# Optimization experiments

Hardware: AMD Instinct MI355X
Metric: run time of the kernel (lower is better)

## Reference

```python
import jax, jax.numpy as jnp
import numpy as np

B, D, H = 1024, 64, 128


def setup_inputs() -> dict:
    key = jax.random.key(0)
    ks = jax.random.split(key, 12)
    s1 = 1.0 / np.sqrt(4 * D)
    sh = 1.0 / np.sqrt(H)
    sd = 1.0 / np.sqrt(D)
    return {
        "x": jax.random.normal(ks[0], (B, D), dtype=jnp.float32),
        # edge_fn: Linear(4D,H) -> ReLU -> Linear(H,H)
        "W1": jax.random.uniform(ks[1], (4 * D, H), minval=-s1, maxval=s1, dtype=jnp.float32),
        "b1": jax.random.uniform(ks[2], (H,), minval=-s1, maxval=s1, dtype=jnp.float32),
        "W2": jax.random.uniform(ks[3], (H, H), minval=-sh, maxval=sh, dtype=jnp.float32),
        "b2": jax.random.uniform(ks[4], (H,), minval=-sh, maxval=sh, dtype=jnp.float32),
        # tau_proj: Linear(D,1) -> Softplus
        "Wt": jax.random.uniform(ks[5], (D, 1), minval=-sd, maxval=sd, dtype=jnp.float32),
        "bt": jax.random.uniform(ks[6], (1,), minval=-sd, maxval=sd, dtype=jnp.float32),
        # agg: Linear(H,H) -> ReLU
        "Wa": jax.random.uniform(ks[7], (H, H), minval=-sh, maxval=sh, dtype=jnp.float32),
        "ba": jax.random.uniform(ks[8], (H,), minval=-sh, maxval=sh, dtype=jnp.float32),
        # res_proj: Linear(D,H)
        "Wr": jax.random.uniform(ks[9], (D, H), minval=-sd, maxval=sd, dtype=jnp.float32),
        "br": jax.random.uniform(ks[10], (H,), minval=-sd, maxval=sd, dtype=jnp.float32),
        # LayerNorm(H)
        "gamma": jnp.ones((H,), dtype=jnp.float32),
        "beta": jnp.zeros((H,), dtype=jnp.float32),
    }


def reference(x, W1, b1, W2, b2, Wt, bt, Wa, ba, Wr, br, gamma, beta):
    d = x.shape[1]
    # Decompose first linear over concat([x_i, x_j, delta, |delta|]) into 4 sub-matmuls;
    # only the |delta| term needs the pairwise [B,B,D] tensor.
    Wi, Wj, Wd, Wab = W1[:d], W1[d:2 * d], W1[2 * d:3 * d], W1[3 * d:]
    ti = x @ Wi            # [B,H] (i-dependent)
    tj = x @ Wj            # [B,H] (j-dependent)
    td = x @ Wd            # [B,H] (delta = x_i - x_j contribution)
    delta = x[:, None, :] - x[None, :, :]             # [B,B,D]
    ta = jnp.einsum('ijd,dh->ijh', jnp.abs(delta), Wab)  # [B,B,H]
    pre = ti[:, None, :] + tj[None, :, :] + td[:, None, :] - td[None, :, :] + ta + b1
    d_proj = jax.nn.relu(pre) @ W2 + b2               # [B,B,H]
    tau = jnp.maximum(jax.nn.softplus(x @ Wt + bt), 0.01) + 1.0  # [B,1]
    h_mean = d_proj.mean(axis=1) / tau                # mean over j
    h = jax.nn.relu(h_mean @ Wa + ba)
    y = h + (x @ Wr + br)
    mu = y.mean(axis=-1, keepdims=True)
    var = ((y - mu) ** 2).mean(axis=-1, keepdims=True)  # biased, like torch LayerNorm
    return (y - mu) * jax.lax.rsqrt(var + 1e-5) * gamma + beta
```

## Files before the change

kernel.cpp:

```cpp
#include <hip/hip_runtime.h>
#include <hip/hip_bf16.h>
#include <math.h>

#define BB 1024
#define DD 64
#define HH 128

typedef __bf16 bf16x8 __attribute__((ext_vector_type(8)));
typedef float floatx4 __attribute__((ext_vector_type(4)));

__device__ __forceinline__ unsigned short f2bf(float v) {
    union { float f; unsigned u; } a; a.f = v;
    unsigned r = a.u + 0x7fffu + ((a.u >> 16) & 1u);
    return (unsigned short)(r >> 16);
}

__device__ __forceinline__ void async_cp16(const float* g, float* lds_wave_base) {
    __builtin_amdgcn_global_load_lds(
        (const __attribute__((address_space(1))) unsigned int*)g,
        (__attribute__((address_space(3))) unsigned int*)lds_wave_base,
        16, 0, 0);
}

__global__ __launch_bounds__(256) void prep_kernel(
    const float* __restrict__ x, const float* __restrict__ W1,
    const float* __restrict__ b1,
    float* __restrict__ c1, float* __restrict__ c2P,
    unsigned short* __restrict__ wpack)
{
    __shared__ float xs[8][DD];
    const int t = threadIdx.x;
    const int i0 = blockIdx.x * 8;
    xs[t >> 6][t & 63] = x[i0 * DD + t];
    xs[4 + (t >> 6)][t & 63] = x[i0 * DD + 256 + t];
    __syncthreads();

    const int ii = t >> 5;
    const int h4 = t & 31;
    const int h = h4 * 4;
    const int i = i0 + ii;

    float4 a1 = {0.f, 0.f, 0.f, 0.f};
    float4 a2 = {0.f, 0.f, 0.f, 0.f};
    #pragma unroll 4
    for (int k = 0; k < DD; k++) {
        float4 wi = *(const float4*)(W1 + k * HH + h);
        float4 wj = *(const float4*)(W1 + (DD + k) * HH + h);
        float4 wd = *(const float4*)(W1 + (2 * DD + k) * HH + h);
        float xv = xs[ii][k];
        a1.x = fmaf(xv, wi.x + wd.x, a1.x);
        a1.y = fmaf(xv, wi.y + wd.y, a1.y);
        a1.z = fmaf(xv, wi.z + wd.z, a1.z);
        a1.w = fmaf(xv, wi.w + wd.w, a1.w);
        a2.x = fmaf(xv, wj.x - wd.x, a2.x);
        a2.y = fmaf(xv, wj.y - wd.y, a2.y);
        a2.z = fmaf(xv, wj.z - wd.z, a2.z);
        a2.w = fmaf(xv, wj.w - wd.w, a2.w);
    }
    float4 b1v = *(const float4*)(b1 + h);
    float4 c1v = {a1.x + b1v.x, a1.y + b1v.y, a1.z + b1v.z, a1.w + b1v.w};
    *(float4*)(c1 + i * HH + h) = c1v;

    const int jl = i & 15;
    float* cb = c2P + (i >> 4) * 2048 + (h >> 4) * 256 + (jl & 3);
    const int p0 = ((jl >> 2) * 16 + (h & 15));
    cb[(p0 + 0) * 4] = a2.x;
    cb[(p0 + 1) * 4] = a2.y;
    cb[(p0 + 2) * 4] = a2.z;
    cb[(p0 + 3) * 4] = a2.w;

    if (blockIdx.x < 64) {
        int f = blockIdx.x * 256 + t;
        int jj = f & 7, l = (f >> 3) & 63, u = f >> 9;
        int s = u & 1, t8 = u >> 1;
        int k = s * 32 + ((l >> 4) << 3) + jj;
        int hh = t8 * 16 + (l & 15);
        wpack[f] = f2bf(W1[(3 * DD + k) * HH + hh]);
    }
}

__global__ __launch_bounds__(256) void pair_kernel(
    const float* __restrict__ x, const float* __restrict__ c1,
    const float* __restrict__ c2P, const unsigned short* __restrict__ wpack,
    float* __restrict__ Sp)
{
    __shared__ __align__(16) float xs[2][1024];
    __shared__ __align__(16) float c2s[2][2048];

    const int t = threadIdx.x;
    const int wave = t >> 6;
    const int l = t & 63;
    const int quad = l >> 4, lm = l & 15;
    const int ig = blockIdx.x >> 2;
    const int jq = blockIdx.x & 3;
    const int i = ig * 4 + wave;
    const int j0base = jq * 256;
    const int sw = lm & 7;

    async_cp16(x + (j0base + (t >> 4)) * DD + (((t & 15) ^ ((t >> 4) & 7)) << 2),
               &xs[0][0] + wave * 256);
    {
        const float* cg = c2P + (j0base >> 4) * 2048;
        async_cp16(cg + t * 4,        &c2s[0][0]    + wave * 256);
        async_cp16(cg + 1024 + t * 4, &c2s[0][1024] + wave * 256);
    }

    float xi[16];
    {
        const float* xg = x + i * DD + quad * 8;
        *(float4*)(xi)      = *(const float4*)(xg);
        *(float4*)(xi + 4)  = *(const float4*)(xg + 4);
        *(float4*)(xi + 8)  = *(const float4*)(xg + 32);
        *(float4*)(xi + 12) = *(const float4*)(xg + 36);
    }
    float c1r[8];
    #pragma unroll
    for (int t8 = 0; t8 < 8; t8++) c1r[t8] = c1[i * HH + t8 * 16 + lm];
    bf16x8 wf[16];
    #pragma unroll
    for (int u = 0; u < 16; u++)
        wf[u] = *(const bf16x8*)(wpack + (u * 64 + l) * 8);

    float S[8];
    #pragma unroll
    for (int t8 = 0; t8 < 8; t8++) S[t8] = 0.f;

    for (int tile = 0; tile < 16; ++tile) {
        const int cur = tile & 1;
        __syncthreads();

        if (tile < 15) {
            const int jn = j0base + (tile + 1) * 16;
            async_cp16(x + (jn + (t >> 4)) * DD + (((t & 15) ^ ((t >> 4) & 7)) << 2),
                       &xs[cur ^ 1][0] + wave * 256);
            const float* cg = c2P + (jn >> 4) * 2048;
            async_cp16(cg + t * 4,        &c2s[cur ^ 1][0]    + wave * 256);
            async_cp16(cg + 1024 + t * 4, &c2s[cur ^ 1][1024] + wave * 256);
        }

        floatx4 acc[8];
        #pragma unroll
        for (int t8 = 0; t8 < 8; t8++) {
            float4 c2v = *(const float4*)(&c2s[cur][t8 * 256 + l * 4]);
            acc[t8][0] = c2v.x + c1r[t8];
            acc[t8][1] = c2v.y + c1r[t8];
            acc[t8][2] = c2v.z + c1r[t8];
            acc[t8][3] = c2v.w + c1r[t8];
        }

        const float* xb = &xs[cur][lm * 64];
        float4 a0 = *(const float4*)(xb + (((quad * 2)     ^ sw) << 2));
        float4 a1 = *(const float4*)(xb + (((quad * 2 + 1) ^ sw) << 2));
        float4 a2 = *(const float4*)(xb + (((quad * 2 + 8) ^ sw) << 2));
        float4 a3 = *(const float4*)(xb + (((quad * 2 + 9) ^ sw) << 2));
        bf16x8 af0, af1;
        af0[0] = (__bf16)fabsf(xi[0] - a0.x);  af0[1] = (__bf16)fabsf(xi[1] - a0.y);
        af0[2] = (__bf16)fabsf(xi[2] - a0.z);  af0[3] = (__bf16)fabsf(xi[3] - a0.w);
        af0[4] = (__bf16)fabsf(xi[4] - a1.x);  af0[5] = (__bf16)fabsf(xi[5] - a1.y);
        af0[6] = (__bf16)fabsf(xi[6] - a1.z);  af0[7] = (__bf16)fabsf(xi[7] - a1.w);
        af1[0] = (__bf16)fabsf(xi[8] - a2.x);  af1[1] = (__bf16)fabsf(xi[9] - a2.y);
        af1[2] = (__bf16)fabsf(xi[10] - a2.z); af1[3] = (__bf16)fabsf(xi[11] - a2.w);
        af1[4] = (__bf16)fabsf(xi[12] - a3.x); af1[5] = (__bf16)fabsf(xi[13] - a3.y);
        af1[6] = (__bf16)fabsf(xi[14] - a3.z); af1[7] = (__bf16)fabsf(xi[15] - a3.w);

        #pragma unroll
        for (int t8 = 0; t8 < 8; t8++) {
            acc[t8] = __builtin_amdgcn_mfma_f32_16x16x32_bf16(af0, wf[t8 * 2 + 0], acc[t8], 0, 0, 0);
            acc[t8] = __builtin_amdgcn_mfma_f32_16x16x32_bf16(af1, wf[t8 * 2 + 1], acc[t8], 0, 0, 0);
        }
        #pragma unroll
        for (int t8 = 0; t8 < 8; t8++) {
            S[t8] += fmaxf(acc[t8][0], 0.f);
            S[t8] += fmaxf(acc[t8][1], 0.f);
            S[t8] += fmaxf(acc[t8][2], 0.f);
            S[t8] += fmaxf(acc[t8][3], 0.f);
        }
    }

    #pragma unroll
    for (int t8 = 0; t8 < 8; t8++) {
        S[t8] += __shfl_xor(S[t8], 16, 64);
        S[t8] += __shfl_xor(S[t8], 32, 64);
    }
    if (quad == 0) {
        #pragma unroll
        for (int t8 = 0; t8 < 8; t8++)
            Sp[(jq * BB + i) * HH + t8 * 16 + lm] = S[t8];
    }
}

__global__ __launch_bounds__(256) void finish_kernel(
    const float* __restrict__ Sp, const float* __restrict__ W2,
    const float* __restrict__ b2, const float* __restrict__ x,
    const float* __restrict__ Wt, const float* __restrict__ bt,
    const float* __restrict__ Wa, const float* __restrict__ ba,
    const float* __restrict__ Wr, const float* __restrict__ br,
    const float* __restrict__ gamma, const float* __restrict__ beta,
    float* __restrict__ out)
{
    __shared__ float Srow[8][HH];
    __shared__ float mrow[8][HH];
    __shared__ float xrow[8][DD];
    __shared__ float taus[8];
    const int t = threadIdx.x;
    const int ii = t >> 5;
    const int h4 = t & 31;
    const int h = h4 * 4;
    const int i0 = blockIdx.x * 8;
    const int i = i0 + ii;

    {
        float4 s = {0.f, 0.f, 0.f, 0.f};
        #pragma unroll
        for (int q = 0; q < 4; q++) {
            float4 v = *(const float4*)(Sp + (q * BB + i) * HH + h);
            s.x += v.x; s.y += v.y; s.z += v.z; s.w += v.w;
        }
        const float inv = 1.0f / (float)BB;
        float4 sm = {s.x * inv, s.y * inv, s.z * inv, s.w * inv};
        *(float4*)(&Srow[ii][h]) = sm;
    }
    xrow[t >> 6][t & 63] = x[i0 * DD + t];
    xrow[4 + (t >> 6)][t & 63] = x[i0 * DD + 256 + t];

    {
        float p = x[i * DD + h4] * Wt[h4] + x[i * DD + 32 + h4] * Wt[32 + h4];
        #pragma unroll
        for (int off = 16; off; off >>= 1) p += __shfl_xor(p, off, 64);
        if (h4 == 0) {
            float z = p + bt[0];
            float sp = (z > 20.f) ? z : log1pf(expf(z));
            taus[ii] = fmaxf(sp, 0.01f) + 1.0f;
        }
    }
    __syncthreads();

    float4 acc = *(const float4*)(b2 + h);
    #pragma unroll 8
    for (int k = 0; k < HH; k++) {
        float4 w = *(const float4*)(W2 + k * HH + h);
        float sv = Srow[ii][k];
        acc.x = fmaf(sv, w.x, acc.x); acc.y = fmaf(sv, w.y, acc.y);
        acc.z = fmaf(sv, w.z, acc.z); acc.w = fmaf(sv, w.w, acc.w);
    }
    const float itau = 1.0f / taus[ii];
    float4 mv = {acc.x * itau, acc.y * itau, acc.z * itau, acc.w * itau};
    *(float4*)(&mrow[ii][h]) = mv;
    __syncthreads();

    float4 a2 = *(const float4*)(ba + h);
    #pragma unroll 8
    for (int k = 0; k < HH; k++) {
        float4 w = *(const float4*)(Wa + k * HH + h);
        float sv = mrow[ii][k];
        a2.x = fmaf(sv, w.x, a2.x); a2.y = fmaf(sv, w.y, a2.y);
        a2.z = fmaf(sv, w.z, a2.z); a2.w = fmaf(sv, w.w, a2.w);
    }
    float4 brv = *(const float4*)(br + h);
    float4 y = {fmaxf(a2.x, 0.f) + brv.x, fmaxf(a2.y, 0.f) + brv.y,
                fmaxf(a2.z, 0.f) + brv.z, fmaxf(a2.w, 0.f) + brv.w};
    #pragma unroll 8
    for (int d = 0; d < DD; d++) {
        float4 w = *(const float4*)(Wr + d * HH + h);
        float xv = xrow[ii][d];
        y.x = fmaf(xv, w.x, y.x); y.y = fmaf(xv, w.y, y.y);
        y.z = fmaf(xv, w.z, y.z); y.w = fmaf(xv, w.w, y.w);
    }

    float p = y.x + y.y + y.z + y.w;
    #pragma unroll
    for (int off = 16; off; off >>= 1) p += __shfl_xor(p, off, 64);
    float mu = p * (1.0f / (float)HH);
    float4 dy = {y.x - mu, y.y - mu, y.z - mu, y.w - mu};
    float q = dy.x * dy.x + dy.y * dy.y + dy.z * dy.z + dy.w * dy.w;
    #pragma unroll
    for (int off = 16; off; off >>= 1) q += __shfl_xor(q, off, 64);
    float rs = rsqrtf(q * (1.0f / (float)HH) + 1e-5f);
    float4 gv = *(const float4*)(gamma + h);
    float4 bv = *(const float4*)(beta + h);
    float4 o = {dy.x * rs * gv.x + bv.x, dy.y * rs * gv.y + bv.y,
                dy.z * rs * gv.z + bv.z, dy.w * rs * gv.w + bv.w};
    *(float4*)(out + i * HH + h) = o;
}

extern "C" void kernel_launch(void* const* d_in, const int* in_sizes, int n_in,
                              void* d_out, int out_size, void* d_ws, size_t ws_size,
                              hipStream_t stream)
{
    const float* x     = (const float*)d_in[0];
    const float* W1    = (const float*)d_in[1];
    const float* b1    = (const float*)d_in[2];
    const float* W2    = (const float*)d_in[3];
    const float* b2    = (const float*)d_in[4];
    const float* Wt    = (const float*)d_in[5];
    const float* bt    = (const float*)d_in[6];
    const float* Wa    = (const float*)d_in[7];
    const float* ba    = (const float*)d_in[8];
    const float* Wr    = (const float*)d_in[9];
    const float* br    = (const float*)d_in[10];
    const float* gamma = (const float*)d_in[11];
    const float* beta  = (const float*)d_in[12];
    float* out = (float*)d_out;

    char* ws = (char*)d_ws;
    float*          c1    = (float*)(ws);
    float*          c2P   = (float*)(ws + (512 << 10));
    unsigned short* wpack = (unsigned short*)(ws + (1024 << 10));
    float*          Sp    = (float*)(ws + (1056 << 10));

    prep_kernel<<<128, 256, 0, stream>>>(x, W1, b1, c1, c2P, wpack);
    pair_kernel<<<1024, 256, 0, stream>>>(x, c1, c2P, wpack, Sp);
    finish_kernel<<<128, 256, 0, stream>>>(Sp, W2, b2, x, Wt, bt,
                                           Wa, ba, Wr, br, gamma, beta, out);
}
```

Measured before the change: 147.8 us.

## Fold j-dependent term into MFMA K dimension and drop LDS staging

Instead of precomputing the j-dependent c2 table and staging it through LDS, the pair kernel now widens the MFMA K dimension from 64 to 128, appending x_j against a packed (Wj - Wd) weight so the j-term is computed inside the matrix core. The block split changes from four j-quarters to two j-halves times two H-halves, and x_j rows are read straight from global into registers with manual double buffering, with no LDS and no barriers. This removes the c2P workspace, its scattered writes, async LDS copies and syncs, at the cost of twice as many MFMAs per output and extra bf16 rounding of the x_j term.

```diff
diff --git a/kernel.cpp b/kernel.cpp
--- a/kernel.cpp
+++ b/kernel.cpp
@@ -15,18 +15,10 @@
     return (unsigned short)(r >> 16);
 }
 
-__device__ __forceinline__ void async_cp16(const float* g, float* lds_wave_base) {
-    __builtin_amdgcn_global_load_lds(
-        (const __attribute__((address_space(1))) unsigned int*)g,
-        (__attribute__((address_space(3))) unsigned int*)lds_wave_base,
-        16, 0, 0);
-}
-
 __global__ __launch_bounds__(256) void prep_kernel(
     const float* __restrict__ x, const float* __restrict__ W1,
     const float* __restrict__ b1,
-    float* __restrict__ c1, float* __restrict__ c2P,
-    unsigned short* __restrict__ wpack)
+    float* __restrict__ c1, unsigned short* __restrict__ wpack)
 {
     __shared__ float xs[8][DD];
     const int t = threadIdx.x;
@@ -41,69 +33,88 @@
     const int i = i0 + ii;
 
     float4 a1 = {0.f, 0.f, 0.f, 0.f};
-    float4 a2 = {0.f, 0.f, 0.f, 0.f};
     #pragma unroll 4
     for (int k = 0; k < DD; k++) {
         float4 wi = *(const float4*)(W1 + k * HH + h);
-        float4 wj = *(const float4*)(W1 + (DD + k) * HH + h);
         float4 wd = *(const float4*)(W1 + (2 * DD + k) * HH + h);
         float xv = xs[ii][k];
         a1.x = fmaf(xv, wi.x + wd.x, a1.x);
         a1.y = fmaf(xv, wi.y + wd.y, a1.y);
         a1.z = fmaf(xv, wi.z + wd.z, a1.z);
         a1.w = fmaf(xv, wi.w + wd.w, a1.w);
-        a2.x = fmaf(xv, wj.x - wd.x, a2.x);
-        a2.y = fmaf(xv, wj.y - wd.y, a2.y);
-        a2.z = fmaf(xv, wj.z - wd.z, a2.z);
-        a2.w = fmaf(xv, wj.w - wd.w, a2.w);
     }
     float4 b1v = *(const float4*)(b1 + h);
     float4 c1v = {a1.x + b1v.x, a1.y + b1v.y, a1.z + b1v.z, a1.w + b1v.w};
     *(float4*)(c1 + i * HH + h) = c1v;
 
-    const int jl = i & 15;
-    float* cb = c2P + (i >> 4) * 2048 + (h >> 4) * 256 + (jl & 3);
-    const int p0 = ((jl >> 2) * 16 + (h & 15));
-    cb[(p0 + 0) * 4] = a2.x;
-    cb[(p0 + 1) * 4] = a2.y;
-    cb[(p0 + 2) * 4] = a2.z;
-    cb[(p0 + 3) * 4] = a2.w;
-
     if (blockIdx.x < 64) {
         int f = blockIdx.x * 256 + t;
-        int jj = f & 7, l = (f >> 3) & 63, u = f >> 9;
-        int s = u & 1, t8 = u >> 1;
-        int k = s * 32 + ((l >> 4) << 3) + jj;
-        int hh = t8 * 16 + (l & 15);
-        wpack[f] = f2bf(W1[(3 * DD + k) * HH + hh]);
-    }
-}
+        int jj = f & 7;
+        int l  = (f >> 3) & 63;
+        int u  = f >> 9;
+        int c  = u & 3, t4 = (u >> 2) & 3, hh = u >> 4;
+        int hcol = hh * 64 + t4 * 16 + (l & 15);
+        float val;
+        if (c < 2) {
+            int k = c * 32 + ((l >> 4) << 3) + jj;
+            val = W1[(3 * DD + k) * HH + hcol];
+        } else {
+            int k = (c - 2) * 32 + ((l >> 4) << 3) + jj;
+            val = W1[(DD + k) * HH + hcol] - W1[(2 * DD + k) * HH + hcol];
+        }
+        wpack[f] = f2bf(val);
+    }
+}
+
+#define LOADT(P0, P1, P2, P3, tile) do {                     \
+    const float* rp_ = xrow + ((tile) & 31) * (16 * DD);     \
+    P0 = *(const float4*)(rp_);                              \
+    P1 = *(const float4*)(rp_ + 4);                          \
+    P2 = *(const float4*)(rp_ + 32);                         \
+    P3 = *(const float4*)(rp_ + 36);                         \
+} while (0)
+
+#define COMPT(A0, A1, A2, A3) do {                                            \
+    bf16x8 af0, af1, af2, af3;                                                \
+    af0[0]=(__bf16)fabsf(xi[0]-A0.x);  af0[1]=(__bf16)fabsf(xi[1]-A0.y);      \
+    af0[2]=(__bf16)fabsf(xi[2]-A0.z);  af0[3]=(__bf16)fabsf(xi[3]-A0.w);      \
+    af0[4]=(__bf16)fabsf(xi[4]-A1.x);  af0[5]=(__bf16)fabsf(xi[5]-A1.y);      \
+    af0[6]=(__bf16)fabsf(xi[6]-A1.z);  af0[7]=(__bf16)fabsf(xi[7]-A1.w);      \
+    af1[0]=(__bf16)fabsf(xi[8]-A2.x);  af1[1]=(__bf16)fabsf(xi[9]-A2.y);      \
+    af1[2]=(__bf16)fabsf(xi[10]-A2.z); af1[3]=(__bf16)fabsf(xi[11]-A2.w);     \
+    af1[4]=(__bf16)fabsf(xi[12]-A3.x); af1[5]=(__bf16)fabsf(xi[13]-A3.y);     \
+    af1[6]=(__bf16)fabsf(xi[14]-A3.z); af1[7]=(__bf16)fabsf(xi[15]-A3.w);     \
+    af2[0]=(__bf16)A0.x; af2[1]=(__bf16)A0.y; af2[2]=(__bf16)A0.z;            \
+    af2[3]=(__bf16)A0.w; af2[4]=(__bf16)A1.x; af2[5]=(__bf16)A1.y;            \
+    af2[6]=(__bf16)A1.z; af2[7]=(__bf16)A1.w;                                 \
+    af3[0]=(__bf16)A2.x; af3[1]=(__bf16)A2.y; af3[2]=(__bf16)A2.z;            \
+    af3[3]=(__bf16)A2.w; af3[4]=(__bf16)A3.x; af3[5]=(__bf16)A3.y;            \
+    af3[6]=(__bf16)A3.z; af3[7]=(__bf16)A3.w;                                 \
+    _Pragma("unroll")                                                         \
+    for (int t4 = 0; t4 < 4; t4++) {                                          \
+        floatx4 acc = {c1r[t4], c1r[t4], c1r[t4], c1r[t4]};                   \
+        acc = __builtin_amdgcn_mfma_f32_16x16x32_bf16(af0, wf[t4*4+0], acc, 0,0,0); \
+        acc = __builtin_amdgcn_mfma_f32_16x16x32_bf16(af1, wf[t4*4+1], acc, 0,0,0); \
+        acc = __builtin_amdgcn_mfma_f32_16x16x32_bf16(af2, wf[t4*4+2], acc, 0,0,0); \
+        acc = __builtin_amdgcn_mfma_f32_16x16x32_bf16(af3, wf[t4*4+3], acc, 0,0,0); \
+        S[t4] += fmaxf(acc[0], 0.f) + fmaxf(acc[1], 0.f)                      \
+               + fmaxf(acc[2], 0.f) + fmaxf(acc[3], 0.f);                     \
+    }                                                                         \
+} while (0)
 
 __global__ __launch_bounds__(256) void pair_kernel(
     const float* __restrict__ x, const float* __restrict__ c1,
-    const float* __restrict__ c2P, const unsigned short* __restrict__ wpack,
-    float* __restrict__ Sp)
-{
-    __shared__ __align__(16) float xs[2][1024];
-    __shared__ __align__(16) float c2s[2][2048];
-
+    const unsigned short* __restrict__ wpack, float* __restrict__ Sp)
+{
     const int t = threadIdx.x;
     const int wave = t >> 6;
     const int l = t & 63;
     const int quad = l >> 4, lm = l & 15;
-    const int ig = blockIdx.x >> 2;
-    const int jq = blockIdx.x & 3;
+    const int bid = blockIdx.x;
+    const int ig = bid >> 2;
+    const int hh = (bid >> 1) & 1;
+    const int jh = bid & 1;
     const int i = ig * 4 + wave;
-    const int j0base = jq * 256;
-    const int sw = lm & 7;
-
-    async_cp16(x + (j0base + (t >> 4)) * DD + (((t & 15) ^ ((t >> 4) & 7)) << 2),
-               &xs[0][0] + wave * 256);
-    {
-        const float* cg = c2P + (j0base >> 4) * 2048;
-        async_cp16(cg + t * 4,        &c2s[0][0]    + wave * 256);
-        async_cp16(cg + 1024 + t * 4, &c2s[0][1024] + wave * 256);
-    }
 
     float xi[16];
     {
@@ -113,79 +124,41 @@
         *(float4*)(xi + 8)  = *(const float4*)(xg + 32);
         *(float4*)(xi + 12) = *(const float4*)(xg + 36);
     }
-    float c1r[8];
-    #pragma unroll
-    for (int t8 = 0; t8 < 8; t8++) c1r[t8] = c1[i * HH + t8 * 16 + lm];
+    float c1r[4];
+    #pragma unroll
+    for (int t4 = 0; t4 < 4; t4++)
+        c1r[t4] = c1[i * HH + hh * 64 + t4 * 16 + lm];
+
     bf16x8 wf[16];
     #pragma unroll
     for (int u = 0; u < 16; u++)
-        wf[u] = *(const bf16x8*)(wpack + (u * 64 + l) * 8);
-
-    float S[8];
-    #pragma unroll
-    for (int t8 = 0; t8 < 8; t8++) S[t8] = 0.f;
-
-    for (int tile = 0; tile < 16; ++tile) {
-        const int cur = tile & 1;
-        __syncthreads();
-
-        if (tile < 15) {
-            const int jn = j0base + (tile + 1) * 16;
-            async_cp16(x + (jn + (t >> 4)) * DD + (((t & 15) ^ ((t >> 4) & 7)) << 2),
-                       &xs[cur ^ 1][0] + wave * 256);
-            const float* cg = c2P + (jn >> 4) * 2048;
-            async_cp16(cg + t * 4,        &c2s[cur ^ 1][0]    + wave * 256);
-            async_cp16(cg + 1024 + t * 4, &c2s[cur ^ 1][1024] + wave * 256);
-        }
-
-        floatx4 acc[8];
-        #pragma unroll
-        for (int t8 = 0; t8 < 8; t8++) {
-            float4 c2v = *(const float4*)(&c2s[cur][t8 * 256 + l * 4]);
-            acc[t8][0] = c2v.x + c1r[t8];
-            acc[t8][1] = c2v.y + c1r[t8];
-            acc[t8][2] = c2v.z + c1r[t8];
-            acc[t8][3] = c2v.w + c1r[t8];
-        }
-
-        const float* xb = &xs[cur][lm * 64];
-        float4 a0 = *(const float4*)(xb + (((quad * 2)     ^ sw) << 2));
-        float4 a1 = *(const float4*)(xb + (((quad * 2 + 1) ^ sw) << 2));
-        float4 a2 = *(const float4*)(xb + (((quad * 2 + 8) ^ sw) << 2));
-        float4 a3 = *(const float4*)(xb + (((quad * 2 + 9) ^ sw) << 2));
-        bf16x8 af0, af1;
-        af0[0] = (__bf16)fabsf(xi[0] - a0.x);  af0[1] = (__bf16)fabsf(xi[1] - a0.y);
-        af0[2] = (__bf16)fabsf(xi[2] - a0.z);  af0[3] = (__bf16)fabsf(xi[3] - a0.w);
-        af0[4] = (__bf16)fabsf(xi[4] - a1.x);  af0[5] = (__bf16)fabsf(xi[5] - a1.y);
-        af0[6] = (__bf16)fabsf(xi[6] - a1.z);  af0[7] = (__bf16)fabsf(xi[7] - a1.w);
-        af1[0] = (__bf16)fabsf(xi[8] - a2.x);  af1[1] = (__bf16)fabsf(xi[9] - a2.y);
-        af1[2] = (__bf16)fabsf(xi[10] - a2.z); af1[3] = (__bf16)fabsf(xi[11] - a2.w);
-        af1[4] = (__bf16)fabsf(xi[12] - a3.x); af1[5] = (__bf16)fabsf(xi[13] - a3.y);
-        af1[6] = (__bf16)fabsf(xi[14] - a3.z); af1[7] = (__bf16)fabsf(xi[15] - a3.w);
-
-        #pragma unroll
-        for (int t8 = 0; t8 < 8; t8++) {
-            acc[t8] = __builtin_amdgcn_mfma_f32_16x16x32_bf16(af0, wf[t8 * 2 + 0], acc[t8], 0, 0, 0);
-            acc[t8] = __builtin_amdgcn_mfma_f32_16x16x32_bf16(af1, wf[t8 * 2 + 1], acc[t8], 0, 0, 0);
-        }
-        #pragma unroll
-        for (int t8 = 0; t8 < 8; t8++) {
-            S[t8] += fmaxf(acc[t8][0], 0.f);
-            S[t8] += fmaxf(acc[t8][1], 0.f);
-            S[t8] += fmaxf(acc[t8][2], 0.f);
-            S[t8] += fmaxf(acc[t8][3], 0.f);
-        }
-    }
-
-    #pragma unroll
-    for (int t8 = 0; t8 < 8; t8++) {
-        S[t8] += __shfl_xor(S[t8], 16, 64);
-        S[t8] += __shfl_xor(S[t8], 32, 64);
+        wf[u] = *(const bf16x8*)(wpack + ((hh * 16 + u) * 64 + l) * 8);
+
+    float S[4] = {0.f, 0.f, 0.f, 0.f};
+
+    const float* xrow = x + (jh * 512 + lm) * DD + quad * 8;
+
+    float4 A0, A1, A2, A3, B0, B1, B2, B3;
+    LOADT(A0, A1, A2, A3, 0);
+    LOADT(B0, B1, B2, B3, 1);
+
+    #pragma unroll 1
+    for (int tp = 0; tp < 32; tp += 2) {
+        COMPT(A0, A1, A2, A3);
+        LOADT(A0, A1, A2, A3, tp + 2);
+        COMPT(B0, B1, B2, B3);
+        LOADT(B0, B1, B2, B3, tp + 3);
+    }
+
+    #pragma unroll
+    for (int t4 = 0; t4 < 4; t4++) {
+        S[t4] += __shfl_xor(S[t4], 16, 64);
+        S[t4] += __shfl_xor(S[t4], 32, 64);
     }
     if (quad == 0) {
         #pragma unroll
-        for (int t8 = 0; t8 < 8; t8++)
-            Sp[(jq * BB + i) * HH + t8 * 16 + lm] = S[t8];
+        for (int t4 = 0; t4 < 4; t4++)
+            Sp[(jh * BB + i) * HH + hh * 64 + t4 * 16 + lm] = S[t4];
     }
 }
 
@@ -200,7 +173,7 @@
 {
     __shared__ float Srow[8][HH];
     __shared__ float mrow[8][HH];
-    __shared__ float xrow[8][DD];
+    __shared__ float xrowS[8][DD];
     __shared__ float taus[8];
     const int t = threadIdx.x;
     const int ii = t >> 5;
@@ -212,7 +185,7 @@
     {
         float4 s = {0.f, 0.f, 0.f, 0.f};
         #pragma unroll
-        for (int q = 0; q < 4; q++) {
+        for (int q = 0; q < 2; q++) {
             float4 v = *(const float4*)(Sp + (q * BB + i) * HH + h);
             s.x += v.x; s.y += v.y; s.z += v.z; s.w += v.w;
         }
@@ -220,8 +193,8 @@
         float4 sm = {s.x * inv, s.y * inv, s.z * inv, s.w * inv};
         *(float4*)(&Srow[ii][h]) = sm;
     }
-    xrow[t >> 6][t & 63] = x[i0 * DD + t];
-    xrow[4 + (t >> 6)][t & 63] = x[i0 * DD + 256 + t];
+    xrowS[t >> 6][t & 63] = x[i0 * DD + t];
+    xrowS[4 + (t >> 6)][t & 63] = x[i0 * DD + 256 + t];
 
     {
         float p = x[i * DD + h4] * Wt[h4] + x[i * DD + 32 + h4] * Wt[32 + h4];
@@ -262,7 +235,7 @@
     #pragma unroll 8
     for (int d = 0; d < DD; d++) {
         float4 w = *(const float4*)(Wr + d * HH + h);
-        float xv = xrow[ii][d];
+        float xv = xrowS[ii][d];
         y.x = fmaf(xv, w.x, y.x); y.y = fmaf(xv, w.y, y.y);
         y.z = fmaf(xv, w.z, y.z); y.w = fmaf(xv, w.w, y.w);
     }
@@ -304,12 +277,11 @@
 
     char* ws = (char*)d_ws;
     float*          c1    = (float*)(ws);
-    float*          c2P   = (float*)(ws + (512 << 10));
-    unsigned short* wpack = (unsigned short*)(ws + (1024 << 10));
-    float*          Sp    = (float*)(ws + (1056 << 10));
-
-    prep_kernel<<<128, 256, 0, stream>>>(x, W1, b1, c1, c2P, wpack);
-    pair_kernel<<<1024, 256, 0, stream>>>(x, c1, c2P, wpack, Sp);
+    unsigned short* wpack = (unsigned short*)(ws + (512 << 10));
+    float*          Sp    = (float*)(ws + (576 << 10));
+
+    prep_kernel<<<128, 256, 0, stream>>>(x, W1, b1, c1, wpack);
+    pair_kernel<<<1024, 256, 0, stream>>>(x, c1, wpack, Sp);
     finish_kernel<<<128, 256, 0, stream>>>(Sp, W2, b2, x, Wt, bt,
                                            Wa, ba, Wr, br, gamma, beta, out);
 }
```

After: 245.2 us. +65.8%, slower.

## Split pair kernel over H halves and switch MFMA operands to fp16

Applied to the files above, without the earlier changes.

The pair kernel grid doubles, and each block now handles half of the hidden dimension. That halves per-thread accumulators, weight fragments and LDS for c2, and occupancy is raised with launch_bounds(256,4). The |delta| operands are packed to fp16 with cvt_pkrtz and use the f16 MFMA instead of the bf16 one with per-element conversions, which cuts conversion cost. In exchange, the x tile loads and abs-difference computation are now done twice, once per H half, and the operands use round-toward-zero fp16 conversion.

```diff
diff --git a/kernel.cpp b/kernel.cpp
--- a/kernel.cpp
+++ b/kernel.cpp
@@ -6,14 +6,11 @@
 #define DD 64
 #define HH 128
 
-typedef __bf16 bf16x8 __attribute__((ext_vector_type(8)));
+typedef _Float16 half8 __attribute__((ext_vector_type(8)));
+typedef __fp16 fp16x2 __attribute__((ext_vector_type(2)));
 typedef float floatx4 __attribute__((ext_vector_type(4)));
 
-__device__ __forceinline__ unsigned short f2bf(float v) {
-    union { float f; unsigned u; } a; a.f = v;
-    unsigned r = a.u + 0x7fffu + ((a.u >> 16) & 1u);
-    return (unsigned short)(r >> 16);
-}
+union H8 { fp16x2 p[4]; half8 v; };
 
 __device__ __forceinline__ void async_cp16(const float* g, float* lds_wave_base) {
     __builtin_amdgcn_global_load_lds(
@@ -26,7 +23,7 @@
     const float* __restrict__ x, const float* __restrict__ W1,
     const float* __restrict__ b1,
     float* __restrict__ c1, float* __restrict__ c2P,
-    unsigned short* __restrict__ wpack)
+    _Float16* __restrict__ wpack)
 {
     __shared__ float xs[8][DD];
     const int t = threadIdx.x;
@@ -62,48 +59,49 @@
     *(float4*)(c1 + i * HH + h) = c1v;
 
     const int jl = i & 15;
-    float* cb = c2P + (i >> 4) * 2048 + (h >> 4) * 256 + (jl & 3);
-    const int p0 = ((jl >> 2) * 16 + (h & 15));
+    float* cb = c2P + (i >> 4) * 2048 + (h >> 6) * 1024 + ((h >> 4) & 3) * 256 + (jl & 3);
+    const int p0 = (jl >> 2) * 16 + (h & 15);
     cb[(p0 + 0) * 4] = a2.x;
     cb[(p0 + 1) * 4] = a2.y;
     cb[(p0 + 2) * 4] = a2.z;
     cb[(p0 + 3) * 4] = a2.w;
 
-    if (blockIdx.x < 64) {
+    if (blockIdx.x < 32) {
         int f = blockIdx.x * 256 + t;
-        int jj = f & 7, l = (f >> 3) & 63, u = f >> 9;
-        int s = u & 1, t8 = u >> 1;
-        int k = s * 32 + ((l >> 4) << 3) + jj;
-        int hh = t8 * 16 + (l & 15);
-        wpack[f] = f2bf(W1[(3 * DD + k) * HH + hh]);
-    }
-}
-
-__global__ __launch_bounds__(256) void pair_kernel(
+        int jj = f & 7;
+        int l  = (f >> 3) & 63;
+        int u  = f >> 9;
+        int s  = u & 1, t4 = (u >> 1) & 3, hh = u >> 3;
+        int k  = s * 32 + ((l >> 4) << 3) + jj;
+        int hcol = hh * 64 + t4 * 16 + (l & 15);
+        wpack[f] = (_Float16)W1[(3 * DD + k) * HH + hcol];
+    }
+}
+
+__global__ __launch_bounds__(256, 4) void pair_kernel(
     const float* __restrict__ x, const float* __restrict__ c1,
-    const float* __restrict__ c2P, const unsigned short* __restrict__ wpack,
+    const float* __restrict__ c2P, const _Float16* __restrict__ wpack,
     float* __restrict__ Sp)
 {
     __shared__ __align__(16) float xs[2][1024];
-    __shared__ __align__(16) float c2s[2][2048];
+    __shared__ __align__(16) float c2s[2][1024];
 
     const int t = threadIdx.x;
     const int wave = t >> 6;
     const int l = t & 63;
     const int quad = l >> 4, lm = l & 15;
-    const int ig = blockIdx.x >> 2;
-    const int jq = blockIdx.x & 3;
+    const int bid = blockIdx.x;
+    const int ig = bid >> 3;
+    const int hh = (bid >> 2) & 1;
+    const int jq = bid & 3;
     const int i = ig * 4 + wave;
     const int j0base = jq * 256;
     const int sw = lm & 7;
 
     async_cp16(x + (j0base + (t >> 4)) * DD + (((t & 15) ^ ((t >> 4) & 7)) << 2),
                &xs[0][0] + wave * 256);
-    {
-        const float* cg = c2P + (j0base >> 4) * 2048;
-        async_cp16(cg + t * 4,        &c2s[0][0]    + wave * 256);
-        async_cp16(cg + 1024 + t * 4, &c2s[0][1024] + wave * 256);
-    }
+    async_cp16(c2P + (j0base >> 4) * 2048 + hh * 1024 + t * 4,
+               &c2s[0][0] + wave * 256);
 
     float xi[16];
     {
@@ -113,17 +111,16 @@
         *(float4*)(xi + 8)  = *(const float4*)(xg + 32);
         *(float4*)(xi + 12) = *(const float4*)(xg + 36);
     }
-    float c1r[8];
-    #pragma unroll
-    for (int t8 = 0; t8 < 8; t8++) c1r[t8] = c1[i * HH + t8 * 16 + lm];
-    bf16x8 wf[16];
-    #pragma unroll
-    for (int u = 0; u < 16; u++)
-        wf[u] = *(const bf16x8*)(wpack + (u * 64 + l) * 8);
-
-    float S[8];
-    #pragma unroll
-    for (int t8 = 0; t8 < 8; t8++) S[t8] = 0.f;
+    float c1r[4];
+    #pragma unroll
+    for (int t4 = 0; t4 < 4; t4++)
+        c1r[t4] = c1[i * HH + hh * 64 + t4 * 16 + lm];
+    half8 wf[8];
+    #pragma unroll
+    for (int u = 0; u < 8; u++)
+        wf[u] = *(const half8*)(wpack + ((hh * 8 + u) * 64 + l) * 8);
+
+    float S[4] = {0.f, 0.f, 0.f, 0.f};
 
     for (int tile = 0; tile < 16; ++tile) {
         const int cur = tile & 1;
@@ -133,19 +130,18 @@
             const int jn = j0base + (tile + 1) * 16;
             async_cp16(x + (jn + (t >> 4)) * DD + (((t & 15) ^ ((t >> 4) & 7)) << 2),
                        &xs[cur ^ 1][0] + wave * 256);
-            const float* cg = c2P + (jn >> 4) * 2048;
-            async_cp16(cg + t * 4,        &c2s[cur ^ 1][0]    + wave * 256);
-            async_cp16(cg + 1024 + t * 4, &c2s[cur ^ 1][1024] + wave * 256);
-        }
-
-        floatx4 acc[8];
-        #pragma unroll
-        for (int t8 = 0; t8 < 8; t8++) {
-            float4 c2v = *(const float4*)(&c2s[cur][t8 * 256 + l * 4]);
-            acc[t8][0] = c2v.x + c1r[t8];
-            acc[t8][1] = c2v.y + c1r[t8];
-            acc[t8][2] = c2v.z + c1r[t8];
-            acc[t8][3] = c2v.w + c1r[t8];
+            async_cp16(c2P + (jn >> 4) * 2048 + hh * 1024 + t * 4,
+                       &c2s[cur ^ 1][0] + wave * 256);
+        }
+
+        floatx4 acc[4];
+        #pragma unroll
+        for (int t4 = 0; t4 < 4; t4++) {
+            float4 c2v = *(const float4*)(&c2s[cur][t4 * 256 + l * 4]);
+            acc[t4][0] = c2v.x + c1r[t4];
+            acc[t4][1] = c2v.y + c1r[t4];
+            acc[t4][2] = c2v.z + c1r[t4];
+            acc[t4][3] = c2v.w + c1r[t4];
         }
 
         const float* xb = &xs[cur][lm * 64];
@@ -153,39 +149,39 @@
         float4 a1 = *(const float4*)(xb + (((quad * 2 + 1) ^ sw) << 2));
         float4 a2 = *(const float4*)(xb + (((quad * 2 + 8) ^ sw) << 2));
         float4 a3 = *(const float4*)(xb + (((quad * 2 + 9) ^ sw) << 2));
-        bf16x8 af0, af1;
-        af0[0] = (__bf16)fabsf(xi[0] - a0.x);  af0[1] = (__bf16)fabsf(xi[1] - a0.y);
-        af0[2] = (__bf16)fabsf(xi[2] - a0.z);  af0[3] = (__bf16)fabsf(xi[3] - a0.w);
-        af0[4] = (__bf16)fabsf(xi[4] - a1.x);  af0[5] = (__bf16)fabsf(xi[5] - a1.y);
-        af0[6] = (__bf16)fabsf(xi[6] - a1.z);  af0[7] = (__bf16)fabsf(xi[7] - a1.w);
-        af1[0] = (__bf16)fabsf(xi[8] - a2.x);  af1[1] = (__bf16)fabsf(xi[9] - a2.y);
-        af1[2] = (__bf16)fabsf(xi[10] - a2.z); af1[3] = (__bf16)fabsf(xi[11] - a2.w);
-        af1[4] = (__bf16)fabsf(xi[12] - a3.x); af1[5] = (__bf16)fabsf(xi[13] - a3.y);
-        af1[6] = (__bf16)fabsf(xi[14] - a3.z); af1[7] = (__bf16)fabsf(xi[15] - a3.w);
-
-        #pragma unroll
-        for (int t8 = 0; t8 < 8; t8++) {
-            acc[t8] = __builtin_amdgcn_mfma_f32_16x16x32_bf16(af0, wf[t8 * 2 + 0], acc[t8], 0, 0, 0);
-            acc[t8] = __builtin_amdgcn_mfma_f32_16x16x32_bf16(af1, wf[t8 * 2 + 1], acc[t8], 0, 0, 0);
-        }
-        #pragma unroll
-        for (int t8 = 0; t8 < 8; t8++) {
-            S[t8] += fmaxf(acc[t8][0], 0.f);
-            S[t8] += fmaxf(acc[t8][1], 0.f);
-            S[t8] += fmaxf(acc[t8][2], 0.f);
-            S[t8] += fmaxf(acc[t8][3], 0.f);
-        }
-    }
-
-    #pragma unroll
-    for (int t8 = 0; t8 < 8; t8++) {
-        S[t8] += __shfl_xor(S[t8], 16, 64);
-        S[t8] += __shfl_xor(S[t8], 32, 64);
+        H8 af0, af1;
+        af0.p[0] = __builtin_amdgcn_cvt_pkrtz(fabsf(xi[0] - a0.x),  fabsf(xi[1] - a0.y));
+        af0.p[1] = __builtin_amdgcn_cvt_pkrtz(fabsf(xi[2] - a0.z),  fabsf(xi[3] - a0.w));
+        af0.p[2] = __builtin_amdgcn_cvt_pkrtz(fabsf(xi[4] - a1.x),  fabsf(xi[5] - a1.y));
+        af0.p[3] = __builtin_amdgcn_cvt_pkrtz(fabsf(xi[6] - a1.z),  fabsf(xi[7] - a1.w));
+        af1.p[0] = __builtin_amdgcn_cvt_pkrtz(fabsf(xi[8] - a2.x),  fabsf(xi[9] - a2.y));
+        af1.p[1] = __builtin_amdgcn_cvt_pkrtz(fabsf(xi[10] - a2.z), fabsf(xi[11] - a2.w));
+        af1.p[2] = __builtin_amdgcn_cvt_pkrtz(fabsf(xi[12] - a3.x), fabsf(xi[13] - a3.y));
+        af1.p[3] = __builtin_amdgcn_cvt_pkrtz(fabsf(xi[14] - a3.z), fabsf(xi[15] - a3.w));
+
+        #pragma unroll
+        for (int t4 = 0; t4 < 4; t4++) {
+            acc[t4] = __builtin_amdgcn_mfma_f32_16x16x32_f16(af0.v, wf[t4 * 2 + 0], acc[t4], 0, 0, 0);
+            acc[t4] = __builtin_amdgcn_mfma_f32_16x16x32_f16(af1.v, wf[t4 * 2 + 1], acc[t4], 0, 0, 0);
+        }
+        #pragma unroll
+        for (int t4 = 0; t4 < 4; t4++) {
+            S[t4] += fmaxf(acc[t4][0], 0.f);
+            S[t4] += fmaxf(acc[t4][1], 0.f);
+            S[t4] += fmaxf(acc[t4][2], 0.f);
+            S[t4] += fmaxf(acc[t4][3], 0.f);
+        }
+    }
+
+    #pragma unroll
+    for (int t4 = 0; t4 < 4; t4++) {
+        S[t4] += __shfl_xor(S[t4], 16, 64);
+        S[t4] += __shfl_xor(S[t4], 32, 64);
     }
     if (quad == 0) {
         #pragma unroll
-        for (int t8 = 0; t8 < 8; t8++)
-            Sp[(jq * BB + i) * HH + t8 * 16 + lm] = S[t8];
+        for (int t4 = 0; t4 < 4; t4++)
+            Sp[(jq * BB + i) * HH + hh * 64 + t4 * 16 + lm] = S[t4];
     }
 }
 
@@ -200,7 +196,7 @@
 {
     __shared__ float Srow[8][HH];
     __shared__ float mrow[8][HH];
-    __shared__ float xrow[8][DD];
+    __shared__ float xrowS[8][DD];
     __shared__ float taus[8];
     const int t = threadIdx.x;
     const int ii = t >> 5;
@@ -220,8 +216,8 @@
         float4 sm = {s.x * inv, s.y * inv, s.z * inv, s.w * inv};
         *(float4*)(&Srow[ii][h]) = sm;
     }
-    xrow[t >> 6][t & 63] = x[i0 * DD + t];
-    xrow[4 + (t >> 6)][t & 63] = x[i0 * DD + 256 + t];
+    xrowS[t >> 6][t & 63] = x[i0 * DD + t];
+    xrowS[4 + (t >> 6)][t & 63] = x[i0 * DD + 256 + t];
 
     {
         float p = x[i * DD + h4] * Wt[h4] + x[i * DD + 32 + h4] * Wt[32 + h4];
@@ -262,7 +258,7 @@
     #pragma unroll 8
     for (int d = 0; d < DD; d++) {
         float4 w = *(const float4*)(Wr + d * HH + h);
-        float xv = xrow[ii][d];
+        float xv = xrowS[ii][d];
         y.x = fmaf(xv, w.x, y.x); y.y = fmaf(xv, w.y, y.y);
         y.z = fmaf(xv, w.z, y.z); y.w = fmaf(xv, w.w, y.w);
     }
@@ -303,13 +299,13 @@
     float* out = (float*)d_out;
 
     char* ws = (char*)d_ws;
-    float*          c1    = (float*)(ws);
-    float*          c2P   = (float*)(ws + (512 << 10));
-    unsigned short* wpack = (unsigned short*)(ws + (1024 << 10));
-    float*          Sp    = (float*)(ws + (1056 << 10));
+    float*     c1    = (float*)(ws);
+    float*     c2P   = (float*)(ws + (512 << 10));
+    _Float16*  wpack = (_Float16*)(ws + (1024 << 10));
+    float*     Sp    = (float*)(ws + (1056 << 10));
 
     prep_kernel<<<128, 256, 0, stream>>>(x, W1, b1, c1, c2P, wpack);
-    pair_kernel<<<1024, 256, 0, stream>>>(x, c1, c2P, wpack, Sp);
+    pair_kernel<<<2048, 256, 0, stream>>>(x, c1, c2P, wpack, Sp);
     finish_kernel<<<128, 256, 0, stream>>>(Sp, W2, b2, x, Wt, bt,
                                            Wa, ba, Wr, br, gamma, beta, out);
 }
```

Measured after the change: 133.7 us. 9.5% less time.
